# Kernel optimization log

Measured on AMD Instinct MI355X. Metric: run time of the kernel, lower is better.

## Reference

```python
import jax, jax.numpy as jnp
import numpy as np

B, N, H, D = 2, 2048, 8, 64  # batch, seq, heads, out_channels (per-head, incl. time dim)
E = H * 64                   # embed dim = num_heads * in_channels
C = 1.0                      # manifold curvature c
EPS = 1e-8


def setup_inputs() -> dict:
    key = jax.random.key(0)
    ks = jax.random.split(key, 8)
    d_out = H * (D - 1)
    inp = {
        "query_input": jax.random.normal(ks[0], (B, N, E), dtype=jnp.float32),
        "source_input": jax.random.normal(ks[1], (B, N, E), dtype=jnp.float32),
        "Wq_w": jax.random.normal(ks[2], (d_out, E), dtype=jnp.float32) * 0.02,
        "Wq_b": jnp.zeros((d_out,), dtype=jnp.float32),
        "Wk_w": jax.random.normal(ks[3], (d_out, E), dtype=jnp.float32) * 0.02,
        "Wk_b": jnp.zeros((d_out,), dtype=jnp.float32),
        "Wv_w": jax.random.normal(ks[4], (d_out, E), dtype=jnp.float32) * 0.02,
        "Wv_b": jnp.zeros((d_out,), dtype=jnp.float32),
        "scale": jnp.array([np.sqrt(H * D)], dtype=jnp.float32),
        "bias": jnp.zeros((), dtype=jnp.float32),
    }
    return inp


def _lift(x_space):
    # project space coords onto hyperboloid: prepend time = sqrt(||x||^2 + c)
    t = jnp.sqrt(jnp.sum(x_space * x_space, axis=-1, keepdims=True) + C)
    return jnp.concatenate([t, x_space], axis=-1)  # [..., D]


def _centroid(ave):
    # Lorentzian centroid normalization: sqrt(c) * ave / sqrt(|<ave,ave>_L|)
    inner = jnp.sum(ave * ave, axis=-1, keepdims=True) - 2.0 * ave[..., :1] ** 2
    denom = jnp.sqrt(jnp.maximum(jnp.abs(inner), EPS))
    return jnp.sqrt(C) * ave / denom


def reference(query_input, source_input, Wq_w, Wq_b, Wk_w, Wk_b, Wv_w, Wv_b, scale, bias):
    def heads(x, W, b):
        return (x @ W.T + b).reshape(B, N, H, D - 1)

    q = _lift(heads(query_input, Wq_w, Wq_b))   # [B,N,H,D]
    k = _lift(heads(source_input, Wk_w, Wk_b))  # [B,N,H,D]
    v = _lift(heads(source_input, Wv_w, Wv_b))  # [B,N,H,D]

    # Lorentzian inner product: negate time component of q
    sign = jnp.concatenate([-jnp.ones((1,), q.dtype), jnp.ones((D - 1,), q.dtype)])
    att = 2.0 * C + 2.0 * jnp.einsum('bnhd,bmhd->bhnm', q * sign, k)  # [B,H,N,N]
    att = att / scale[0] + bias
    w = jax.nn.softmax(att, axis=-1)

    ave = jnp.einsum('bhnm,bmhd->bnhd', w, v)   # weighted sum of values
    out = _centroid(ave)                         # per-head hyperbolic centroid [B,N,H,D]
    out = _centroid(jnp.mean(out, axis=2))       # centroid across heads -> [B,N,D]
    return out
```

## Files before the change

### kernel.cpp

```cpp
#include <hip/hip_runtime.h>
#include <math.h>
#include <stdint.h>

#define BB   2
#define NN   2048
#define HH   8
#define DD   64
#define EE   512
#define DM1  63

typedef _Float16 half8  __attribute__((ext_vector_type(8)));
typedef __fp16   fp16x2 __attribute__((ext_vector_type(2)));
typedef float    floatx4 __attribute__((ext_vector_type(4)));

__device__ __forceinline__ uint32_t pkh2(float a, float b) {
    union { fp16x2 h; uint32_t u; } uu;
    uu.h = __builtin_amdgcn_cvt_pkrtz(a, b);
    return uu.u;
}

__global__ __launch_bounds__(256, 3) void qkv_mfma(
    const float* __restrict__ Xq, const float* __restrict__ Xs,
    const float* __restrict__ Wq, const float* __restrict__ Wk,
    const float* __restrict__ Wv,
    const float* __restrict__ Wqb, const float* __restrict__ Wkb,
    const float* __restrict__ Wvb, const float* __restrict__ scale_p,
    _Float16* __restrict__ q16, _Float16* __restrict__ k16,
    _Float16* __restrict__ vT16)
{
    const int mtb = blockIdx.x;
    const int hp  = blockIdx.y;
    const int mat = blockIdx.z;
    const int t    = threadIdx.x;
    const int w    = t >> 6;
    const int lane = t & 63;
    const int l15  = lane & 15;
    const int quad = lane >> 4;

    __shared__ alignas(16) char smem[27648];
    __shared__ float psum[64][4];
    _Float16 (*Xsh)[72]  = (_Float16(*)[72])smem;
    _Float16 (*Wsh)[72]  = (_Float16(*)[72])(smem + 9216);
    _Float16 (*Osh)[136] = (_Float16(*)[136])(smem + 9216);
    _Float16 (*OshT)[72] = (_Float16(*)[72])(smem + 9216);

    const float* X    = (mat == 0) ? Xq : Xs;
    const float* W    = (mat == 0) ? Wq : (mat == 1 ? Wk : Wv);
    const float* bias = (mat == 0) ? Wqb : (mat == 1 ? Wkb : Wvb);
    const int tok0 = mtb * 64;

    floatx4 acc[4][2];
#pragma unroll
    for (int mt = 0; mt < 4; mt++)
#pragma unroll
        for (int nt = 0; nt < 2; nt++) acc[mt][nt] = (floatx4){0.f,0.f,0.f,0.f};

    float4 pxa[2], pxb[2], pwa[4], pwb[4];
#pragma unroll
    for (int ls = 0; ls < 2; ls++) {
        int g = t + 256 * ls, r = g >> 3, c = g & 7;
        const float* p = X + (size_t)(tok0 + r) * EE + c * 8;
        pxa[ls] = *(const float4*)p;
        pxb[ls] = *(const float4*)(p + 4);
    }
#pragma unroll
    for (int ls = 0; ls < 4; ls++) {
        int g = t + 256 * ls, r = g >> 3, c = g & 7;
        int head = r >> 6, j = r & 63;
        pwa[ls] = make_float4(0.f,0.f,0.f,0.f);
        pwb[ls] = make_float4(0.f,0.f,0.f,0.f);
        if (j < DM1) {
            const float* p = W + (size_t)((hp * 2 + head) * DM1 + j) * EE + c * 8;
            pwa[ls] = *(const float4*)p;
            pwb[ls] = *(const float4*)(p + 4);
        }
    }

    for (int it = 0; it < 8; it++) {
        __syncthreads();
#pragma unroll
        for (int ls = 0; ls < 2; ls++) {
            int g = t + 256 * ls, r = g >> 3, c = g & 7;
            uint4 h;
            h.x = pkh2(pxa[ls].x, pxa[ls].y); h.y = pkh2(pxa[ls].z, pxa[ls].w);
            h.z = pkh2(pxb[ls].x, pxb[ls].y); h.w = pkh2(pxb[ls].z, pxb[ls].w);
            *(uint4*)&Xsh[r][c * 8] = h;
        }
#pragma unroll
        for (int ls = 0; ls < 4; ls++) {
            int g = t + 256 * ls, r = g >> 3, c = g & 7;
            uint4 h;
            h.x = pkh2(pwa[ls].x, pwa[ls].y); h.y = pkh2(pwa[ls].z, pwa[ls].w);
            h.z = pkh2(pwb[ls].x, pwb[ls].y); h.w = pkh2(pwb[ls].z, pwb[ls].w);
            *(uint4*)&Wsh[r][c * 8] = h;
        }
        __syncthreads();
        if (it + 1 < 8) {
            int ek = (it + 1) * 64;
#pragma unroll
            for (int ls = 0; ls < 2; ls++) {
                int g = t + 256 * ls, r = g >> 3, c = g & 7;
                const float* p = X + (size_t)(tok0 + r) * EE + ek + c * 8;
                pxa[ls] = *(const float4*)p;
                pxb[ls] = *(const float4*)(p + 4);
            }
#pragma unroll
            for (int ls = 0; ls < 4; ls++) {
                int g = t + 256 * ls, r = g >> 3, c = g & 7;
                int head = r >> 6, j = r & 63;
                if (j < DM1) {
                    const float* p = W + (size_t)((hp * 2 + head) * DM1 + j) * EE + ek + c * 8;
                    pwa[ls] = *(const float4*)p;
                    pwb[ls] = *(const float4*)(p + 4);
                }
            }
        }
#pragma unroll
        for (int kk = 0; kk < 2; kk++) {
            half8 a[4];
#pragma unroll
            for (int mt = 0; mt < 4; mt++)
                a[mt] = *(const half8*)&Xsh[mt * 16 + l15][kk * 32 + quad * 8];
#pragma unroll
            for (int nt = 0; nt < 2; nt++) {
                half8 bfr = *(const half8*)&Wsh[w * 32 + nt * 16 + l15][kk * 32 + quad * 8];
#pragma unroll
                for (int mt = 0; mt < 4; mt++)
                    acc[mt][nt] = __builtin_amdgcn_mfma_f32_16x16x32_f16(
                        a[mt], bfr, acc[mt][nt], 0, 0, 0);
            }
        }
    }
    __syncthreads();

    const float st   = 2.0f / scale_p[0];
    const float fmul = (mat == 0) ? st : 1.0f;

    float vals[4][2][4];
    float sqp[4][4];
#pragma unroll
    for (int mt = 0; mt < 4; mt++)
#pragma unroll
        for (int r = 0; r < 4; r++) sqp[mt][r] = 0.f;

#pragma unroll
    for (int mt = 0; mt < 4; mt++)
#pragma unroll
        for (int nt = 0; nt < 2; nt++) {
            int col = w * 32 + nt * 16 + l15;
            int head = col >> 6, j = col & 63;
            float bb = (j < DM1) ? bias[(hp * 2 + head) * DM1 + j] : 0.f;
#pragma unroll
            for (int r = 0; r < 4; r++) {
                float vv = acc[mt][nt][r] + bb;
                if (j >= DM1) vv = 0.f;
                vals[mt][nt][r] = vv;
                sqp[mt][r] += vv * vv;
            }
        }
#pragma unroll
    for (int mt = 0; mt < 4; mt++)
#pragma unroll
        for (int r = 0; r < 4; r++) {
            float s = sqp[mt][r];
            s += __shfl_xor(s, 1, 64); s += __shfl_xor(s, 2, 64);
            s += __shfl_xor(s, 4, 64); s += __shfl_xor(s, 8, 64);
            if (l15 == 0) psum[mt * 16 + quad * 4 + r][w] = s;
        }

    if (mat < 2) {
#pragma unroll
        for (int mt = 0; mt < 4; mt++)
#pragma unroll
            for (int nt = 0; nt < 2; nt++) {
                int col = w * 32 + nt * 16 + l15;
                int head = col >> 6, j = col & 63;
                if (j < DM1) {
                    int dc = head * 64 + 1 + j;
#pragma unroll
                    for (int r = 0; r < 4; r++)
                        Osh[mt * 16 + quad * 4 + r][dc] = (_Float16)(vals[mt][nt][r] * fmul);
                }
            }
    } else {
#pragma unroll
        for (int mt = 0; mt < 4; mt++)
#pragma unroll
            for (int nt = 0; nt < 2; nt++) {
                int col = w * 32 + nt * 16 + l15;
                uint2 pu;
                pu.x = pkh2(vals[mt][nt][0], vals[mt][nt][1]);
                pu.y = pkh2(vals[mt][nt][2], vals[mt][nt][3]);
                *(uint2*)&OshT[col][mt * 16 + quad * 4] = pu;
            }
    }
    __syncthreads();
    if (t < 64) {
        float tsA = sqrtf(psum[t][0] + psum[t][1] + 1.0f);
        float tsB = sqrtf(psum[t][2] + psum[t][3] + 1.0f);
        if (mat < 2) {
            float tm = (mat == 0) ? -st : 1.0f;
            Osh[t][0]  = (_Float16)(tsA * tm);
            Osh[t][64] = (_Float16)(tsB * tm);
        } else {
            OshT[63][t]  = (_Float16)tsA;
            OshT[127][t] = (_Float16)tsB;
        }
    }
    __syncthreads();

    const int bI = tok0 >> 11, n0 = tok0 & 2047;
    if (mat < 2) {
        _Float16* O = (mat == 0) ? q16 : k16;
#pragma unroll
        for (int ls = 0; ls < 4; ls++) {
            int s = t + 256 * ls, r = s >> 4, c = s & 15, head = c >> 3;
            size_t bh = (size_t)(bI * HH + hp * 2 + head);
            *(uint4*)&O[(bh * NN + n0 + r) * DD + (c & 7) * 8] = *(const uint4*)&Osh[r][c * 8];
        }
    } else {
#pragma unroll
        for (int ls = 0; ls < 4; ls++) {
            int s = t + 256 * ls, df = s >> 3, c = s & 7;
            int head = df >> 6, d = df & 63;
            int rr = head * 64 + ((d + 63) & 63);
            size_t bh = (size_t)(bI * HH + hp * 2 + head);
            *(uint4*)&vT16[(bh * DD + d) * NN + n0 + c * 8] = *(const uint4*)&OshT[rr][c * 8];
        }
    }
}

__global__ __launch_bounds__(256, 2) void lorentz_attn_v9(
    const _Float16* __restrict__ q16, const _Float16* __restrict__ k16,
    const _Float16* __restrict__ vT16,
    _Float16* __restrict__ Odh, float* __restrict__ Ors)
{
    const int qt = blockIdx.x;
    const int bh = blockIdx.y;
    const int ks = blockIdx.z;
    const int t    = threadIdx.x;
    const int w    = t >> 6;
    const int lane = t & 63;
    const int l15  = lane & 15;
    const int quad = lane >> 4;

    __shared__ alignas(16) char smem[73728];
    _Float16 (*Psw)[72] = (_Float16(*)[72])(smem + 36864 + w * 9216);

    const _Float16* kb = k16  + (size_t)bh * NN * DD;
    const _Float16* vb = vT16 + (size_t)bh * DD * NN;
    const int kt0 = ks * 8;

    half8 qb[4][2];
#pragma unroll
    for (int mt = 0; mt < 4; mt++) {
        const _Float16* qrow = q16 +
            ((size_t)bh * NN + qt * 256 + w * 64 + mt * 16 + l15) * DD;
        qb[mt][0] = *(const half8*)&qrow[quad * 8];
        qb[mt][1] = *(const half8*)&qrow[32 + quad * 8];
    }

    half8 vones;
#pragma unroll
    for (int i = 0; i < 8; i++) vones[i] = (_Float16)1.0f;

    uint4 pk[2], pv[2];
#pragma unroll
    for (int ls = 0; ls < 2; ls++) {
        int s = t + 256 * ls, r = s >> 3, c = s & 7;
        pk[ls] = *(const uint4*)&kb[((size_t)kt0 * 64 + r) * DD + c * 8];
        pv[ls] = *(const uint4*)&vb[(size_t)r * NN + kt0 * 64 + c * 8];
    }
#pragma unroll
    for (int ls = 0; ls < 2; ls++) {
        int s = t + 256 * ls, r = s >> 3, c = s & 7;
        *(uint4*)(smem +         (size_t)r * 144 + c * 16) = pk[ls];
        *(uint4*)(smem + 18432 + (size_t)r * 144 + c * 16) = pv[ls];
    }
    __syncthreads();

    floatx4 oacc[4][5];
#pragma unroll
    for (int mt = 0; mt < 4; mt++)
#pragma unroll
        for (int nt = 0; nt < 5; nt++) oacc[mt][nt] = (floatx4){0.f,0.f,0.f,0.f};

    for (int i = 0; i < 8; i++) {
        const int kt = kt0 + i;
        const int buf = i & 1;
        _Float16 (*Ks)[72]  = (_Float16(*)[72])(smem + buf * 9216);
        _Float16 (*VTs)[72] = (_Float16(*)[72])(smem + 18432 + buf * 9216);

        if (i + 1 < 8) {
#pragma unroll
            for (int ls = 0; ls < 2; ls++) {
                int s = t + 256 * ls, r = s >> 3, c = s & 7;
                pk[ls] = *(const uint4*)&kb[((size_t)(kt + 1) * 64 + r) * DD + c * 8];
                pv[ls] = *(const uint4*)&vb[(size_t)r * NN + (kt + 1) * 64 + c * 8];
            }
        }

#pragma unroll
        for (int nt = 0; nt < 4; nt++) {
            floatx4 sacc[4];
#pragma unroll
            for (int mt = 0; mt < 4; mt++) sacc[mt] = (floatx4){0.f,0.f,0.f,0.f};
#pragma unroll
            for (int kk = 0; kk < 2; kk++) {
                half8 kf = *(const half8*)&Ks[nt * 16 + l15][kk * 32 + quad * 8];
#pragma unroll
                for (int mt = 0; mt < 4; mt++)
                    sacc[mt] = __builtin_amdgcn_mfma_f32_16x16x32_f16(
                        kf, qb[mt][kk], sacc[mt], 0, 0, 0);
            }
#pragma unroll
            for (int mt = 0; mt < 4; mt++) {
                uint2 pu;
                pu.x = pkh2(__expf(sacc[mt][0]), __expf(sacc[mt][1]));
                pu.y = pkh2(__expf(sacc[mt][2]), __expf(sacc[mt][3]));
                *(uint2*)&Psw[mt * 16 + l15][nt * 16 + quad * 4] = pu;
            }
        }

#pragma unroll
        for (int kk = 0; kk < 2; kk++) {
            half8 pa[4];
#pragma unroll
            for (int mt = 0; mt < 4; mt++)
                pa[mt] = *(const half8*)&Psw[mt * 16 + l15][kk * 32 + quad * 8];
#pragma unroll
            for (int nt = 0; nt < 4; nt++) {
                half8 vf = *(const half8*)&VTs[nt * 16 + l15][kk * 32 + quad * 8];
#pragma unroll
                for (int mt = 0; mt < 4; mt++)
                    oacc[mt][nt] = __builtin_amdgcn_mfma_f32_16x16x32_f16(
                        pa[mt], vf, oacc[mt][nt], 0, 0, 0);
            }
#pragma unroll
            for (int mt = 0; mt < 4; mt++)
                oacc[mt][4] = __builtin_amdgcn_mfma_f32_16x16x32_f16(
                    pa[mt], vones, oacc[mt][4], 0, 0, 0);
        }

        if (i + 1 < 8) {
            char* kd = smem +         (1 - buf) * 9216;
            char* vd = smem + 18432 + (1 - buf) * 9216;
#pragma unroll
            for (int ls = 0; ls < 2; ls++) {
                int s = t + 256 * ls, r = s >> 3, c = s & 7;
                *(uint4*)(kd + (size_t)r * 144 + c * 16) = pk[ls];
                *(uint4*)(vd + (size_t)r * 144 + c * 16) = pv[ls];
            }
        }
        __syncthreads();
    }

    const size_t obase = (((size_t)ks * 16 + bh) * NN + qt * 256 + w * 64);
    float* slab = (float*)Psw;
#pragma unroll
    for (int mt = 0; mt < 4; mt++) {
#pragma unroll
        for (int nt = 0; nt < 4; nt++)
#pragma unroll
            for (int r = 0; r < 4; r++)
                slab[(quad * 4 + r) * 68 + nt * 16 + l15] = oacc[mt][nt][r];
#pragma unroll
        for (int i = 0; i < 4; i++) {
            int s = lane + 64 * i, row = s >> 4, c4 = (s & 15) * 4;
            float4 v = *(const float4*)&slab[row * 68 + c4];
            uint2 pu;
            pu.x = pkh2(v.x, v.y);
            pu.y = pkh2(v.z, v.w);
            *(uint2*)&Odh[(obase + mt * 16 + row) * 64 + c4] = pu;
        }
        if (l15 == 0) {
#pragma unroll
            for (int r = 0; r < 4; r++)
                Ors[obase + mt * 16 + quad * 4 + r] = oacc[mt][4][r];
        }
    }
}

__global__ __launch_bounds__(256) void merge_centroid(
    const _Float16* __restrict__ Odh, const float* __restrict__ Ors,
    float* __restrict__ out)
{
    const int t    = threadIdx.x;
    const int tok  = blockIdx.x * 4 + (t >> 6);
    const int lane = t & 63;
    const int b = tok >> 11;
    const int n = tok & 2047;

    float m = 0.f;
#pragma unroll
    for (int h = 0; h < HH; h++) {
        const size_t bh = (size_t)(b * HH + h);
        float o = 0.f, rs = 0.f;
#pragma unroll
        for (int ksp = 0; ksp < 4; ksp++) {
            const size_t row = ((size_t)ksp * 16 + bh) * NN + n;
            o  += (float)Odh[row * 64 + lane];
            rs += Ors[row];
        }
        float a  = o / rs;
        float ssq = a * a;
#pragma unroll
        for (int off = 32; off > 0; off >>= 1)
            ssq += __shfl_xor(ssq, off, 64);
        float a0 = __shfl(a, 0, 64);
        float inner = ssq - 2.0f * a0 * a0;
        float f = rsqrtf(fmaxf(fabsf(inner), 1e-8f));
        m += a * f;
    }
    m *= 0.125f;

    float sq = m * m;
#pragma unroll
    for (int off = 32; off > 0; off >>= 1)
        sq += __shfl_xor(sq, off, 64);
    float m0 = __shfl(m, 0, 64);
    float inner = sq - 2.0f * m0 * m0;
    float f = rsqrtf(fmaxf(fabsf(inner), 1e-8f));
    out[(size_t)tok * DD + lane] = m * f;
}

extern "C" void kernel_launch(void* const* d_in, const int* in_sizes, int n_in,
                              void* d_out, int out_size, void* d_ws, size_t ws_size,
                              hipStream_t stream)
{
    const float* Xq  = (const float*)d_in[0];
    const float* Xs  = (const float*)d_in[1];
    const float* Wq  = (const float*)d_in[2];
    const float* Wqb = (const float*)d_in[3];
    const float* Wk  = (const float*)d_in[4];
    const float* Wkb = (const float*)d_in[5];
    const float* Wv  = (const float*)d_in[6];
    const float* Wvb = (const float*)d_in[7];
    const float* sc  = (const float*)d_in[8];
    float* out = (float*)d_out;

    const size_t QSZ = (size_t)BB * HH * NN * DD;
    _Float16* q16  = (_Float16*)d_ws;
    _Float16* k16  = q16 + QSZ;
    _Float16* vT16 = k16 + QSZ;
    _Float16* Odh  = vT16 + QSZ;
    float* Ors = (float*)(Odh + (size_t)4 * 16 * NN * 64);

    qkv_mfma<<<dim3(64, 4, 3), 256, 0, stream>>>(Xq, Xs, Wq, Wk, Wv,
                                                 Wqb, Wkb, Wvb, sc,
                                                 q16, k16, vT16);
    lorentz_attn_v9<<<dim3(8, 16, 4), 256, 0, stream>>>(q16, k16, vT16, Odh, Ors);
    merge_centroid<<<(BB * NN) / 4, 256, 0, stream>>>(Odh, Ors, out);
}
```

Before: 129.7 us.

## Keep P in registers via permuted V layout, raise occupancy and key splits

```diff
diff --git a/kernel.cpp b/kernel.cpp
--- a/kernel.cpp
+++ b/kernel.cpp
@@ -8,6 +8,7 @@
 #define DD   64
 #define EE   512
 #define DM1  63
+#define KSP  6
 
 typedef _Float16 half8  __attribute__((ext_vector_type(8)));
 typedef __fp16   fp16x2 __attribute__((ext_vector_type(2)));
@@ -17,6 +18,9 @@
     union { fp16x2 h; uint32_t u; } uu;
     uu.h = __builtin_amdgcn_cvt_pkrtz(a, b);
     return uu.u;
+}
+__device__ __forceinline__ half8 as_half8(uint4 u) {
+    union { uint4 u; half8 h; } uu; uu.u = u; return uu.h;
 }
 
 __global__ __launch_bounds__(256, 3) void qkv_mfma(
@@ -225,12 +229,18 @@
             int head = df >> 6, d = df & 63;
             int rr = head * 64 + ((d + 63) & 63);
             size_t bh = (size_t)(bI * HH + hp * 2 + head);
-            *(uint4*)&vT16[(bh * DD + d) * NN + n0 + c * 8] = *(const uint4*)&OshT[rr][c * 8];
-        }
-    }
-}
-
-__global__ __launch_bounds__(256, 2) void lorentz_attn_v9(
+            uint4 v = *(const uint4*)&OshT[rr][c * 8];
+            int cc = c & 3, hf = c >> 2;
+            int sA = hf * 32 + ((2 * cc) & 3) * 8 + (cc >> 1) * 4;
+            int sB = hf * 32 + ((2 * cc + 1) & 3) * 8 + (cc >> 1) * 4;
+            _Float16* vrow = &vT16[(bh * DD + d) * NN + n0];
+            *(uint2*)&vrow[sA] = make_uint2(v.x, v.y);
+            *(uint2*)&vrow[sB] = make_uint2(v.z, v.w);
+        }
+    }
+}
+
+__global__ __launch_bounds__(256, 3) void lorentz_attn_v10(
     const _Float16* __restrict__ q16, const _Float16* __restrict__ k16,
     const _Float16* __restrict__ vT16,
     _Float16* __restrict__ Odh, float* __restrict__ Ors)
@@ -244,12 +254,12 @@
     const int l15  = lane & 15;
     const int quad = lane >> 4;
 
-    __shared__ alignas(16) char smem[73728];
-    _Float16 (*Psw)[72] = (_Float16(*)[72])(smem + 36864 + w * 9216);
+    __shared__ alignas(16) char smem[36864];
 
     const _Float16* kb = k16  + (size_t)bh * NN * DD;
     const _Float16* vb = vT16 + (size_t)bh * DD * NN;
-    const int kt0 = ks * 8;
+    const int base = (ks < 2) ? ks * 6 : 12 + (ks - 2) * 5;
+    const int cnt  = (ks < 2) ? 6 : 5;
 
     half8 qb[4][2];
 #pragma unroll
@@ -268,8 +278,8 @@
 #pragma unroll
     for (int ls = 0; ls < 2; ls++) {
         int s = t + 256 * ls, r = s >> 3, c = s & 7;
-        pk[ls] = *(const uint4*)&kb[((size_t)kt0 * 64 + r) * DD + c * 8];
-        pv[ls] = *(const uint4*)&vb[(size_t)r * NN + kt0 * 64 + c * 8];
+        pk[ls] = *(const uint4*)&kb[((size_t)base * 64 + r) * DD + c * 8];
+        pv[ls] = *(const uint4*)&vb[(size_t)r * NN + base * 64 + c * 8];
     }
 #pragma unroll
     for (int ls = 0; ls < 2; ls++) {
@@ -285,13 +295,13 @@
 #pragma unroll
         for (int nt = 0; nt < 5; nt++) oacc[mt][nt] = (floatx4){0.f,0.f,0.f,0.f};
 
-    for (int i = 0; i < 8; i++) {
-        const int kt = kt0 + i;
+    for (int i = 0; i < cnt; i++) {
+        const int kt = base + i;
         const int buf = i & 1;
         _Float16 (*Ks)[72]  = (_Float16(*)[72])(smem + buf * 9216);
         _Float16 (*VTs)[72] = (_Float16(*)[72])(smem + 18432 + buf * 9216);
 
-        if (i + 1 < 8) {
+        if (i + 1 < cnt) {
 #pragma unroll
             for (int ls = 0; ls < 2; ls++) {
                 int s = t + 256 * ls, r = s >> 3, c = s & 7;
@@ -301,36 +311,35 @@
         }
 
 #pragma unroll
-        for (int nt = 0; nt < 4; nt++) {
-            floatx4 sacc[4];
-#pragma unroll
-            for (int mt = 0; mt < 4; mt++) sacc[mt] = (floatx4){0.f,0.f,0.f,0.f};
-#pragma unroll
-            for (int kk = 0; kk < 2; kk++) {
-                half8 kf = *(const half8*)&Ks[nt * 16 + l15][kk * 32 + quad * 8];
-#pragma unroll
-                for (int mt = 0; mt < 4; mt++)
-                    sacc[mt] = __builtin_amdgcn_mfma_f32_16x16x32_f16(
-                        kf, qb[mt][kk], sacc[mt], 0, 0, 0);
-            }
+        for (int half = 0; half < 2; half++) {
+            floatx4 sacc[2][4];
+#pragma unroll
+            for (int nt2 = 0; nt2 < 2; nt2++) {
+#pragma unroll
+                for (int mt = 0; mt < 4; mt++) sacc[nt2][mt] = (floatx4){0.f,0.f,0.f,0.f};
+                const int nt = half * 2 + nt2;
+#pragma unroll
+                for (int kk = 0; kk < 2; kk++) {
+                    half8 kf = *(const half8*)&Ks[nt * 16 + l15][kk * 32 + quad * 8];
+#pragma unroll
+                    for (int mt = 0; mt < 4; mt++)
+                        sacc[nt2][mt] = __builtin_amdgcn_mfma_f32_16x16x32_f16(
+                            kf, qb[mt][kk], sacc[nt2][mt], 0, 0, 0);
+                }
+            }
+            half8 pa[4];
 #pragma unroll
             for (int mt = 0; mt < 4; mt++) {
-                uint2 pu;
-                pu.x = pkh2(__expf(sacc[mt][0]), __expf(sacc[mt][1]));
-                pu.y = pkh2(__expf(sacc[mt][2]), __expf(sacc[mt][3]));
-                *(uint2*)&Psw[mt * 16 + l15][nt * 16 + quad * 4] = pu;
-            }
-        }
-
-#pragma unroll
-        for (int kk = 0; kk < 2; kk++) {
-            half8 pa[4];
-#pragma unroll
-            for (int mt = 0; mt < 4; mt++)
-                pa[mt] = *(const half8*)&Psw[mt * 16 + l15][kk * 32 + quad * 8];
+                uint4 u;
+                u.x = pkh2(__expf(sacc[0][mt][0]), __expf(sacc[0][mt][1]));
+                u.y = pkh2(__expf(sacc[0][mt][2]), __expf(sacc[0][mt][3]));
+                u.z = pkh2(__expf(sacc[1][mt][0]), __expf(sacc[1][mt][1]));
+                u.w = pkh2(__expf(sacc[1][mt][2]), __expf(sacc[1][mt][3]));
+                pa[mt] = as_half8(u);
+            }
 #pragma unroll
             for (int nt = 0; nt < 4; nt++) {
-                half8 vf = *(const half8*)&VTs[nt * 16 + l15][kk * 32 + quad * 8];
+                half8 vf = *(const half8*)&VTs[nt * 16 + l15][half * 32 + quad * 8];
 #pragma unroll
                 for (int mt = 0; mt < 4; mt++)
                     oacc[mt][nt] = __builtin_amdgcn_mfma_f32_16x16x32_f16(
@@ -342,7 +351,7 @@
                     pa[mt], vones, oacc[mt][4], 0, 0, 0);
         }
 
-        if (i + 1 < 8) {
+        if (i + 1 < cnt) {
             char* kd = smem +         (1 - buf) * 9216;
             char* vd = smem + 18432 + (1 - buf) * 9216;
 #pragma unroll
@@ -356,7 +365,7 @@
     }
 
     const size_t obase = (((size_t)ks * 16 + bh) * NN + qt * 256 + w * 64);
-    float* slab = (float*)Psw;
+    float* slab = (float*)(smem + w * 4608);
 #pragma unroll
     for (int mt = 0; mt < 4; mt++) {
 #pragma unroll
@@ -397,7 +406,7 @@
         const size_t bh = (size_t)(b * HH + h);
         float o = 0.f, rs = 0.f;
 #pragma unroll
-        for (int ksp = 0; ksp < 4; ksp++) {
+        for (int ksp = 0; ksp < KSP; ksp++) {
             const size_t row = ((size_t)ksp * 16 + bh) * NN + n;
             o  += (float)Odh[row * 64 + lane];
             rs += Ors[row];
@@ -444,11 +453,11 @@
     _Float16* k16  = q16 + QSZ;
     _Float16* vT16 = k16 + QSZ;
     _Float16* Odh  = vT16 + QSZ;
-    float* Ors = (float*)(Odh + (size_t)4 * 16 * NN * 64);
+    float* Ors = (float*)(Odh + (size_t)KSP * 16 * NN * 64);
 
     qkv_mfma<<<dim3(64, 4, 3), 256, 0, stream>>>(Xq, Xs, Wq, Wk, Wv,
                                                  Wqb, Wkb, Wvb, sc,
                                                  q16, k16, vT16);
-    lorentz_attn_v9<<<dim3(8, 16, 4), 256, 0, stream>>>(q16, k16, vT16, Odh, Ors);
+    lorentz_attn_v10<<<dim3(8, 16, KSP), 256, 0, stream>>>(q16, k16, vT16, Odh, Ors);
     merge_centroid<<<(BB * NN) / 4, 256, 0, stream>>>(Odh, Ors, out);
 }
```

Measured after the change: 147.2 us. +13.5%, slower.
